# Kernel optimization log

Hardware: AMD Instinct MI355X
Metric: run time of the kernel (lower is better)

Reference implementation:

```python
import jax, jax.numpy as jnp
import numpy as np

B, T, D = 4, 2048, 1024
N_HEADS = 16
D_HEAD = D // N_HEADS


def setup_inputs() -> dict:
    key = jax.random.key(0)
    ks = jax.random.split(key, 5)
    s = 1.0 / np.sqrt(D)  # keep activations well-scaled
    return {
        "x": jax.random.normal(ks[0], (B, T, D), dtype=jnp.float32),
        "Wq": jax.random.normal(ks[1], (D, D), dtype=jnp.float32) * s,
        "Wk": jax.random.normal(ks[2], (D, D), dtype=jnp.float32) * s,
        "Wv": jax.random.normal(ks[3], (D, D), dtype=jnp.float32) * s,
        "Wo": jax.random.normal(ks[4], (D, D), dtype=jnp.float32) * s,
    }


def reference(x, Wq, Wk, Wv, Wo):
    Bx, Tx, C = x.shape
    # projections; nn.Linear(d,d,bias=False): y = x @ W^T
    def split_heads(y):
        return y.reshape(Bx, Tx, N_HEADS, D_HEAD).transpose(0, 2, 1, 3)  # [B,H,T,dh]
    q = split_heads(x @ Wq.T)
    k = split_heads(x @ Wk.T)
    v = split_heads(x @ Wv.T)
    scale = 1.0 / np.sqrt(D_HEAD)
    att = jnp.einsum("bhtd,bhsd->bhts", q, k) * scale  # [B,H,T,T]
    causal = jnp.tril(jnp.ones((Tx, Tx), dtype=bool))
    att = jnp.where(causal[None, None], att, -jnp.inf)
    att = jax.nn.softmax(att, axis=-1)
    y = jnp.einsum("bhts,bhsd->bhtd", att, v)  # [B,H,T,dh]
    y = y.transpose(0, 2, 1, 3).reshape(Bx, Tx, C)
    return y @ Wo.T
```

## Files before the change

### kernel.cpp

```cpp
#include <hip/hip_runtime.h>
#include <cstdint>
#include <cstddef>

typedef unsigned short u16;
typedef short bf16x8 __attribute__((ext_vector_type(8)));
typedef unsigned short u16x8 __attribute__((ext_vector_type(8)));
typedef float f32x4 __attribute__((ext_vector_type(4)));
typedef float f32x16 __attribute__((ext_vector_type(16)));
typedef unsigned u32x2 __attribute__((ext_vector_type(2)));

__device__ __forceinline__ u16 f2bf(float x) {
    union { float f; unsigned int u; } v; v.f = x;
    unsigned int u = v.u;
    unsigned int r = (u + 0x7fffu + ((u >> 16) & 1u)) >> 16;
    return (u16)r;
}

__device__ __forceinline__ unsigned cvtpk(float lo, float hi) {
    unsigned r;
    asm("v_cvt_pk_bf16_f32 %0, %1, %2" : "=v"(r) : "v"(lo), "v"(hi));
    return r;
}

__device__ __forceinline__ float exp2v(float x) {
    float y;
    asm("v_exp_f32 %0, %1" : "=v"(y) : "v"(x));
    return y;
}

__device__ __forceinline__ void load_lds16(const void* g, void* l) {
    __builtin_amdgcn_global_load_lds((const __attribute__((address_space(1))) void*)g,
                                     (__attribute__((address_space(3))) void*)l, 16, 0, 0);
}

__global__ void cast_f32_bf16(const float* __restrict__ in, u16* __restrict__ out, int n) {
    int i = (blockIdx.x * blockDim.x + threadIdx.x) * 4;
    int stride = gridDim.x * blockDim.x * 4;
    for (; i < n; i += stride) {
        float4 f = *reinterpret_cast<const float4*>(in + i);
        ushort4 o;
        o.x = f2bf(f.x); o.y = f2bf(f.y); o.z = f2bf(f.z); o.w = f2bf(f.w);
        *reinterpret_cast<ushort4*>(out + i) = o;
    }
}

__global__ void cast_w4(const float* __restrict__ w0, const float* __restrict__ w1,
                        const float* __restrict__ w2, const float* __restrict__ w3,
                        u16* __restrict__ out, int nw) {
    const int wsel = blockIdx.y;
    const float* in = (wsel == 0) ? w0 : (wsel == 1) ? w1 : (wsel == 2) ? w2 : w3;
    u16* o = out + (size_t)wsel * nw;
    int i = (blockIdx.x * blockDim.x + threadIdx.x) * 4;
    int stride = gridDim.x * blockDim.x * 4;
    for (; i < nw; i += stride) {
        float4 f = *reinterpret_cast<const float4*>(in + i);
        ushort4 v;
        v.x = f2bf(f.x); v.y = f2bf(f.y); v.z = f2bf(f.z); v.w = f2bf(f.w);
        *reinterpret_cast<ushort4*>(o + i) = v;
    }
}

__global__ __launch_bounds__(512, 2) void gemm_qkv(const u16* __restrict__ A,
                                                   const u16* __restrict__ Bw,
                                                   u16* __restrict__ qkout,
                                                   u16* __restrict__ vtg) {
    constexpr int K = 1024, NT = 32;
    __shared__ u16 smem[49152];

    const int tid  = threadIdx.x;
    const int m0   = blockIdx.x * 256;
    const int n0   = blockIdx.y * 256;
    const int wid  = tid >> 6, lane = tid & 63;
    const int fr   = lane & 15, g = lane >> 4;
    const int wm   = wid >> 2, wn = wid & 3;

    const int r0   = tid >> 2;
    const int ssrc = (tid & 3) ^ ((r0 >> 1) & 3);
    const int wb   = (tid & ~63) * 8;
    const u16* pA0 = A  + (size_t)(m0 + r0) * K + ssrc * 8;
    const u16* pA1 = A  + (size_t)(m0 + r0 + 128) * K + ssrc * 8;
    const u16* pB0 = Bw + (size_t)(n0 + r0) * K + ssrc * 8;
    const u16* pB1 = Bw + (size_t)(n0 + r0 + 128) * K + ssrc * 8;

    int offA[8], offB[4];
#pragma unroll
    for (int mf = 0; mf < 8; ++mf) {
        const int row = wm * 128 + mf * 16 + fr;
        offA[mf] = row * 32 + (g ^ ((row >> 1) & 3)) * 8;
    }
#pragma unroll
    for (int nfr = 0; nfr < 4; ++nfr) {
        const int row = wn * 64 + nfr * 16 + fr;
        offB[nfr] = 8192 + row * 32 + (g ^ ((row >> 1) & 3)) * 8;
    }

    f32x4 acc[8][4];
#pragma unroll
    for (int i = 0; i < 8; ++i)
#pragma unroll
        for (int j = 0; j < 4; ++j) acc[i][j] = f32x4{0.f, 0.f, 0.f, 0.f};

#define ISSUE(BUF) {                                                   \
        load_lds16(pA0, &smem[(BUF) * 16384 + wb]);                    \
        load_lds16(pA1, &smem[(BUF) * 16384 + 4096 + wb]);             \
        load_lds16(pB0, &smem[(BUF) * 16384 + 8192 + wb]);             \
        load_lds16(pB1, &smem[(BUF) * 16384 + 12288 + wb]);            \
        pA0 += 32; pA1 += 32; pB0 += 32; pB1 += 32; }

    ISSUE(0);
    ISSUE(1);

    int b = 0;
    for (int t = 0; t < NT; ++t) {
        if (t < NT - 1) asm volatile("s_waitcnt vmcnt(4)\n\ts_barrier" ::: "memory");
        else            asm volatile("s_waitcnt vmcnt(0)\n\ts_barrier" ::: "memory");

        if (t + 2 < NT) {
            const int b2 = (b == 0) ? 2 : b - 1;
            ISSUE(b2);
        }

        const u16* Tb = &smem[b * 16384];
        bf16x8 a[8], bv[4];
#pragma unroll
        for (int mf = 0; mf < 8; ++mf)
            a[mf] = *reinterpret_cast<const bf16x8*>(&Tb[offA[mf]]);
#pragma unroll
        for (int nfr = 0; nfr < 4; ++nfr)
            bv[nfr] = *reinterpret_cast<const bf16x8*>(&Tb[offB[nfr]]);

        __builtin_amdgcn_s_setprio(1);
#pragma unroll
        for (int mf = 0; mf < 8; ++mf)
#pragma unroll
            for (int nfr = 0; nfr < 4; ++nfr)
                acc[mf][nfr] = __builtin_amdgcn_mfma_f32_16x16x32_bf16(
                    a[mf], bv[nfr], acc[mf][nfr], 0, 0, 0);
        __builtin_amdgcn_s_setprio(0);

        b = (b == 2) ? 0 : b + 1;
    }
#undef ISSUE

    __syncthreads();

    char* sb = reinterpret_cast<char*>(smem);
    if (n0 < 2048) {
        const float osc = (n0 < 1024) ? 0.18033688011112042f : 1.0f;
#pragma unroll
        for (int half = 0; half < 2; ++half) {
            if (wm == half) {
#pragma unroll
                for (int mf = 0; mf < 8; ++mf)
#pragma unroll
                    for (int nfr = 0; nfr < 4; ++nfr) {
                        const int rl  = mf * 16 + g * 4;
                        const int col = wn * 64 + nfr * 16 + fr;
#pragma unroll
                        for (int i = 0; i < 4; ++i) {
                            const int row  = rl + i;
                            const int byte = row * 512 + ((col * 2) ^ (((row >> 2) & 3) << 5));
                            *reinterpret_cast<u16*>(sb + byte) = f2bf(acc[mf][nfr][i] * osc);
                        }
                    }
            }
            __syncthreads();
            {
                const int row = tid >> 2;
                const int swz = ((row >> 2) & 3) << 5;
#pragma unroll
                for (int p = 0; p < 8; ++p) {
                    const int sl   = (tid & 3) + p * 4;
                    const int byte = row * 512 + ((sl * 16) ^ swz);
                    u16x8 v = *reinterpret_cast<const u16x8*>(sb + byte);
                    *reinterpret_cast<u16x8*>(
                        &qkout[(size_t)(m0 + half * 128 + row) * 2048 + n0 + sl * 8]) = v;
                }
            }
            __syncthreads();
        }
    } else {
        const int bb = m0 >> 11, tloc = m0 & 2047;
#pragma unroll
        for (int half = 0; half < 2; ++half) {
            if ((wn >> 1) == half) {
#pragma unroll
                for (int mf = 0; mf < 8; ++mf)
#pragma unroll
                    for (int nfr = 0; nfr < 4; ++nfr) {
                        const int nl  = (wn & 1) * 64 + nfr * 16 + fr;
                        const int ml0 = wm * 128 + mf * 16 + g * 4;
                        const int f   = ((nl & 3) << 5) | (((nl >> 2) & 1) << 4);
                        uint2 pk;
                        pk.x = cvtpk(acc[mf][nfr][0], acc[mf][nfr][1]);
                        pk.y = cvtpk(acc[mf][nfr][2], acc[mf][nfr][3]);
                        *reinterpret_cast<uint2*>(sb + nl * 512 + ((ml0 * 2) ^ f)) = pk;
                    }
            }
            __syncthreads();
            {
                const int nl = tid >> 2;
                const int f  = ((nl & 3) << 5) | (((nl >> 2) & 1) << 4);
#pragma unroll
                for (int p = 0; p < 8; ++p) {
                    const int sl   = (tid & 3) + p * 4;
                    const int byte = nl * 512 + ((sl * 16) ^ f);
                    u16x8 v = *reinterpret_cast<const u16x8*>(sb + byte);
                    *reinterpret_cast<u16x8*>(
                        &vtg[(size_t)(bb * 1024 + (n0 - 2048) + half * 128 + nl) * 2048 +
                             tloc + sl * 8]) = v;
                }
            }
            __syncthreads();
        }
    }
}

__global__ __launch_bounds__(256) void gemm_out(const u16* __restrict__ A,
                                                const u16* __restrict__ Bw,
                                                float* __restrict__ C,
                                                int M, int N, int K) {
    __shared__ u16 smem[16384];
    u16* As = smem;
    u16* Bs = smem + 4096;

    const int tid  = threadIdx.x;
    const int m0   = blockIdx.x * 128;
    const int n0   = blockIdx.y * 128;
    const int wid  = tid >> 6;
    const int lane = tid & 63;
    const int wr   = (wid >> 1) * 64;
    const int wc   = (wid & 1) * 64;
    const int fr   = lane & 15;
    const int ko   = (lane >> 4) * 8;
    const int rq   = (lane >> 4) * 4;

    f32x4 acc[4][4];
#pragma unroll
    for (int i = 0; i < 4; ++i)
#pragma unroll
        for (int j = 0; j < 4; ++j) acc[i][j] = f32x4{0.f, 0.f, 0.f, 0.f};

    const int lr4 = lane >> 2;
    const int ls  = lane & 3;

    for (int k0 = 0; k0 < K; k0 += 32) {
#pragma unroll
        for (int t = 0; t < 2; ++t) {
            const int qtr = wid * 2 + t;
            const int r   = qtr * 16 + lr4;
            load_lds16(&A[(size_t)(m0 + r) * K + k0 + ls * 8], &As[qtr * 512]);
            load_lds16(&Bw[(size_t)(n0 + r) * K + k0 + ls * 8], &Bs[qtr * 512]);
        }
        __syncthreads();

        bf16x8 af[4], bfr[4];
#pragma unroll
        for (int mf = 0; mf < 4; ++mf)
            af[mf] = *reinterpret_cast<const bf16x8*>(&As[(wr + mf * 16 + fr) * 32 + ko]);
#pragma unroll
        for (int nf = 0; nf < 4; ++nf)
            bfr[nf] = *reinterpret_cast<const bf16x8*>(&Bs[(wc + nf * 16 + fr) * 32 + ko]);
        __builtin_amdgcn_s_setprio(1);
#pragma unroll
        for (int mf = 0; mf < 4; ++mf)
#pragma unroll
            for (int nf = 0; nf < 4; ++nf)
                acc[mf][nf] = __builtin_amdgcn_mfma_f32_16x16x32_bf16(
                    af[mf], bfr[nf], acc[mf][nf], 0, 0, 0);
        __builtin_amdgcn_s_setprio(0);
        __syncthreads();
    }

#pragma unroll
    for (int mf = 0; mf < 4; ++mf)
#pragma unroll
        for (int nf = 0; nf < 4; ++nf)
#pragma unroll
            for (int i = 0; i < 4; ++i)
                C[(size_t)(m0 + wr + mf * 16 + rq + i) * N + n0 + wc + nf * 16 + fr] =
                    acc[mf][nf][i];
}

__global__ __launch_bounds__(128) void attn_fwd(const u16* __restrict__ qk,
                                                const u16* __restrict__ vtg,
                                                u16* __restrict__ Y) {
    constexpr int T = 2048, DQK = 2048, DOUT = 1024;
    const int bh = blockIdx.x;
    const int jb = blockIdx.y;
    const int b  = bh >> 4, hd = bh & 15;
    const int tid = threadIdx.x, w = tid >> 6, lane = tid & 63;
    const int qloc = lane & 31, h2 = lane >> 5;

    __shared__ u16 Ks[2][4096];
    __shared__ u16 Vs[2][4096];

    const size_t rowb = (size_t)b * T;
    const int sr8 = lane >> 3, ss = lane & 7;
    const int sc = (ss ^ sr8) * 8;

#define BUILD_PA(sv, RB, dst) {                                               \
        unsigned wa  = cvtpk(sv[RB + 0], sv[RB + 1]);                         \
        unsigned wb2 = cvtpk(sv[RB + 2], sv[RB + 3]);                         \
        unsigned wc2 = cvtpk(sv[RB + 4], sv[RB + 5]);                         \
        unsigned wd  = cvtpk(sv[RB + 6], sv[RB + 7]);                         \
        u32x2 r0 = __builtin_amdgcn_permlane32_swap(wa, wc2, false, false);   \
        u32x2 r1 = __builtin_amdgcn_permlane32_swap(wb2, wd, false, false);   \
        dst.x = r0.x; dst.y = r1.x; dst.z = r0.y; dst.w = r1.y; }

#define PV_STEP(pa, KS, ROWBASE, oacc) {                                      \
        const int rr_ = (ROWBASE) + qloc;                                     \
        bf16x8 vf_ = *reinterpret_cast<const bf16x8*>(                        \
            &Vb[rr_ * 64 + (((2 * (KS) + h2) ^ (rr_ & 7)) * 8)]);             \
        oacc = __builtin_amdgcn_mfma_f32_32x32x16_bf16(                       \
            *reinterpret_cast<const bf16x8*>(&pa), vf_, oacc, 0, 0, 0); }

    for (int qi = 0; qi < 2; ++qi) {
        const int qt = (qi == 0) ? (31 - jb) : jb;
        const int q0 = qt * 64;
        const int wq = q0 + w * 32;
        const int NT = qt + 1;

        bf16x8 qf[4];
#pragma unroll
        for (int ks = 0; ks < 4; ++ks)
            qf[ks] = *reinterpret_cast<const bf16x8*>(
                &qk[(rowb + wq + qloc) * DQK + hd * 64 + ks * 16 + h2 * 8]);

        f32x16 o0, o1;
#pragma unroll
        for (int i = 0; i < 16; ++i) { o0[i] = 0.f; o1[i] = 0.f; }
        float lp = 0.f;

        const u16* kp[4];
        const u16* vp[4];
#pragma unroll
        for (int t = 0; t < 4; ++t) {
            const int r = (w * 4 + t) * 8 + sr8;
            kp[t] = qk + (rowb + r) * DQK + 1024 + hd * 64 + sc;
            vp[t] = vtg + ((size_t)bh * 64 + r) * T + sc;
        }

        __syncthreads();

#pragma unroll
        for (int t = 0; t < 4; ++t) {
            const int chunk = w * 4 + t;
            load_lds16(kp[t], &Ks[0][chunk * 512]);
            load_lds16(vp[t], &Vs[0][chunk * 512]);
        }
#pragma unroll
        for (int t = 0; t < 4; ++t) { kp[t] += 64 * DQK; vp[t] += 64; }

        for (int kt = 0; kt < NT; ++kt) {
            __syncthreads();

            if (kt + 1 < NT) {
                const int nb = (kt + 1) & 1;
#pragma unroll
                for (int t = 0; t < 4; ++t) {
                    const int chunk = w * 4 + t;
                    load_lds16(kp[t], &Ks[nb][chunk * 512]);
                    load_lds16(vp[t], &Vs[nb][chunk * 512]);
                }
#pragma unroll
                for (int t = 0; t < 4; ++t) { kp[t] += 64 * DQK; vp[t] += 64; }
            }

            const int k0 = kt * 64;
            if (k0 <= wq + 31) {
                const u16* Kb = Ks[kt & 1];
                const u16* Vb = Vs[kt & 1];
                const bool do1 = (k0 + 32 <= wq + 31);
                const bool dm  = (k0 + 63 > wq);

                f32x16 st0, st1;
#pragma unroll
                for (int i = 0; i < 16; ++i) { st0[i] = 0.f; st1[i] = 0.f; }

                __builtin_amdgcn_s_setprio(1);
#pragma unroll
                for (int ks = 0; ks < 4; ++ks) {
                    bf16x8 kf = *reinterpret_cast<const bf16x8*>(
                        &Kb[qloc * 64 + (((2 * ks + h2) ^ (qloc & 7)) * 8)]);
                    st0 = __builtin_amdgcn_mfma_f32_32x32x16_bf16(kf, qf[ks], st0, 0, 0, 0);
                }
                if (do1) {
#pragma unroll
                    for (int ks = 0; ks < 4; ++ks) {
                        const int r1 = 32 + qloc;
                        bf16x8 kf = *reinterpret_cast<const bf16x8*>(
                            &Kb[r1 * 64 + (((2 * ks + h2) ^ (r1 & 7)) * 8)]);
                        st1 = __builtin_amdgcn_mfma_f32_32x32x16_bf16(kf, qf[ks], st1, 0, 0, 0);
                    }
                }
                __builtin_amdgcn_s_setprio(0);

                const int qg = wq + qloc;
#pragma unroll
                for (int i = 0; i < 16; ++i) st0[i] = exp2v(st0[i]);
                if (do1) {
#pragma unroll
                    for (int i = 0; i < 16; ++i) st1[i] = exp2v(st1[i]);
                }
                if (dm) {
#pragma unroll
                    for (int r = 0; r < 16; ++r) {
                        const int crow = (r & 3) + 8 * (r >> 2) + 4 * h2;
                        if (k0 + crow > qg)      st0[r] = 0.f;
                        if (k0 + 32 + crow > qg) st1[r] = 0.f;
                    }
                }
                {
                    float l0 = 0.f, l1 = 0.f, l2 = 0.f, l3 = 0.f;
#pragma unroll
                    for (int i = 0; i < 4; ++i) {
                        l0 += st0[i]; l1 += st0[4 + i]; l2 += st0[8 + i]; l3 += st0[12 + i];
                    }
                    if (do1) {
#pragma unroll
                        for (int i = 0; i < 4; ++i) {
                            l0 += st1[i]; l1 += st1[4 + i]; l2 += st1[8 + i]; l3 += st1[12 + i];
                        }
                    }
                    lp += (l0 + l1) + (l2 + l3);
                }

                uint4 pa0, pa1, pa2, pa3;
                BUILD_PA(st0, 0, pa0);
                BUILD_PA(st0, 8, pa1);
                if (do1) {
                    BUILD_PA(st1, 0, pa2);
                    BUILD_PA(st1, 8, pa3);
                }

                __builtin_amdgcn_s_setprio(1);
                PV_STEP(pa0, 0, 0, o0);
                PV_STEP(pa1, 1, 0, o0);
                PV_STEP(pa0, 0, 32, o1);
                PV_STEP(pa1, 1, 32, o1);
                if (do1) {
                    PV_STEP(pa2, 2, 0, o0);
                    PV_STEP(pa3, 3, 0, o0);
                    PV_STEP(pa2, 2, 32, o1);
                    PV_STEP(pa3, 3, 32, o1);
                }
                __builtin_amdgcn_s_setprio(0);
            }
        }

        const float lf = lp + __shfl_xor(lp, 32);
        const float linv = 1.0f / lf;
#pragma unroll
        for (int r = 0; r < 16; ++r) {
            const int crow = (r & 3) + 8 * (r >> 2) + 4 * h2;
            const float rl = __shfl(linv, crow);
            const size_t yrow = rowb + wq + crow;
            Y[yrow * DOUT + hd * 64 + qloc]      = (u16)cvtpk(o0[r] * rl, 0.f);
            Y[yrow * DOUT + hd * 64 + 32 + qloc] = (u16)cvtpk(o1[r] * rl, 0.f);
        }
    }
#undef BUILD_PA
#undef PV_STEP
}

extern "C" void kernel_launch(void* const* d_in, const int* in_sizes, int n_in,
                              void* d_out, int out_size, void* d_ws, size_t ws_size,
                              hipStream_t stream) {
    const float* x  = (const float*)d_in[0];
    const float* Wq = (const float*)d_in[1];
    const float* Wk = (const float*)d_in[2];
    const float* Wv = (const float*)d_in[3];
    const float* Wo = (const float*)d_in[4];

    constexpr int B = 4, T = 2048, D = 1024;
    constexpr int M = B * T;
    const int nx = in_sizes[0];
    const int nw = in_sizes[1];

    char* ws = (char*)d_ws;
    u16* xb   = (u16*)(ws);
    u16* qkb  = (u16*)(ws + (16ull << 20));
    u16* vtg  = (u16*)(ws + (48ull << 20));
    u16* yb   = (u16*)(ws + (64ull << 20));
    u16* wqkv = (u16*)(ws + (80ull << 20));
    u16* wob  = wqkv + 3 * (size_t)nw;

    cast_f32_bf16<<<2048, 256, 0, stream>>>(x, xb, nx);
    cast_w4<<<dim3(256, 4), 256, 0, stream>>>(Wq, Wk, Wv, Wo, wqkv, nw);

    gemm_qkv<<<dim3(M / 256, 3072 / 256), 512, 0, stream>>>(xb, wqkv, qkb, vtg);

    attn_fwd<<<dim3(64, 16), 128, 0, stream>>>(qkb, vtg, yb);

    gemm_out<<<dim3(M / 128, D / 128), 256, 0, stream>>>(yb, wob, (float*)d_out, M, D, D);
}
```

Measured before the change: 169.6 us.

## Enlarge attention query tile to 256 rows with 8 waves sharing K/V tiles

```diff
diff --git a/kernel.cpp b/kernel.cpp
--- a/kernel.cpp
+++ b/kernel.cpp
@@ -282,7 +282,7 @@
                     acc[mf][nf][i];
 }
 
-__global__ __launch_bounds__(128) void attn_fwd(const u16* __restrict__ qk,
+__global__ __launch_bounds__(512) void attn_fwd(const u16* __restrict__ qk,
                                                 const u16* __restrict__ vtg,
                                                 u16* __restrict__ Y) {
     constexpr int T = 2048, DQK = 2048, DOUT = 1024;
@@ -296,8 +296,15 @@
     __shared__ u16 Vs[2][4096];
 
     const size_t rowb = (size_t)b * T;
-    const int sr8 = lane >> 3, ss = lane & 7;
-    const int sc = (ss ^ sr8) * 8;
+
+    const int srow = tid >> 3;
+    const int sc   = ((tid & 7) ^ (srow & 7)) * 8;
+    const int ldst = w * 512;
+
+    int off[4];
+#pragma unroll
+    for (int ks = 0; ks < 4; ++ks)
+        off[ks] = qloc * 64 + (((2 * ks + h2) ^ (qloc & 7)) * 8);
 
 #define BUILD_PA(sv, RB, dst) {                                               \
         unsigned wa  = cvtpk(sv[RB + 0], sv[RB + 1]);                         \
@@ -308,18 +315,16 @@
         u32x2 r1 = __builtin_amdgcn_permlane32_swap(wb2, wd, false, false);   \
         dst.x = r0.x; dst.y = r1.x; dst.z = r0.y; dst.w = r1.y; }
 
-#define PV_STEP(pa, KS, ROWBASE, oacc) {                                      \
-        const int rr_ = (ROWBASE) + qloc;                                     \
-        bf16x8 vf_ = *reinterpret_cast<const bf16x8*>(                        \
-            &Vb[rr_ * 64 + (((2 * (KS) + h2) ^ (rr_ & 7)) * 8)]);             \
+#define PV_STEP(pa, KS, RBOFF, oacc) {                                        \
+        bf16x8 vf_ = *reinterpret_cast<const bf16x8*>(&Vb[off[KS] + (RBOFF)]); \
         oacc = __builtin_amdgcn_mfma_f32_32x32x16_bf16(                       \
             *reinterpret_cast<const bf16x8*>(&pa), vf_, oacc, 0, 0, 0); }
 
     for (int qi = 0; qi < 2; ++qi) {
-        const int qt = (qi == 0) ? (31 - jb) : jb;
-        const int q0 = qt * 64;
+        const int qt = (qi == 0) ? (7 - jb) : jb;
+        const int q0 = qt * 256;
         const int wq = q0 + w * 32;
-        const int NT = qt + 1;
+        const int NT = 4 * qt + 4;
 
         bf16x8 qf[4];
 #pragma unroll
@@ -332,39 +337,23 @@
         for (int i = 0; i < 16; ++i) { o0[i] = 0.f; o1[i] = 0.f; }
         float lp = 0.f;
 
-        const u16* kp[4];
-        const u16* vp[4];
-#pragma unroll
-        for (int t = 0; t < 4; ++t) {
-            const int r = (w * 4 + t) * 8 + sr8;
-            kp[t] = qk + (rowb + r) * DQK + 1024 + hd * 64 + sc;
-            vp[t] = vtg + ((size_t)bh * 64 + r) * T + sc;
-        }
+        const u16* kp = qk  + (rowb + srow) * DQK + 1024 + hd * 64 + sc;
+        const u16* vp = vtg + ((size_t)bh * 64 + srow) * T + sc;
 
         __syncthreads();
 
-#pragma unroll
-        for (int t = 0; t < 4; ++t) {
-            const int chunk = w * 4 + t;
-            load_lds16(kp[t], &Ks[0][chunk * 512]);
-            load_lds16(vp[t], &Vs[0][chunk * 512]);
-        }
-#pragma unroll
-        for (int t = 0; t < 4; ++t) { kp[t] += 64 * DQK; vp[t] += 64; }
+        load_lds16(kp, &Ks[0][ldst]);
+        load_lds16(vp, &Vs[0][ldst]);
+        kp += 64 * DQK; vp += 64;
 
         for (int kt = 0; kt < NT; ++kt) {
             __syncthreads();
 
             if (kt + 1 < NT) {
                 const int nb = (kt + 1) & 1;
-#pragma unroll
-                for (int t = 0; t < 4; ++t) {
-                    const int chunk = w * 4 + t;
-                    load_lds16(kp[t], &Ks[nb][chunk * 512]);
-                    load_lds16(vp[t], &Vs[nb][chunk * 512]);
-                }
-#pragma unroll
-                for (int t = 0; t < 4; ++t) { kp[t] += 64 * DQK; vp[t] += 64; }
+                load_lds16(kp, &Ks[nb][ldst]);
+                load_lds16(vp, &Vs[nb][ldst]);
+                kp += 64 * DQK; vp += 64;
             }
 
             const int k0 = kt * 64;
@@ -381,16 +370,13 @@
                 __builtin_amdgcn_s_setprio(1);
 #pragma unroll
                 for (int ks = 0; ks < 4; ++ks) {
-                    bf16x8 kf = *reinterpret_cast<const bf16x8*>(
-                        &Kb[qloc * 64 + (((2 * ks + h2) ^ (qloc & 7)) * 8)]);
+                    bf16x8 kf = *reinterpret_cast<const bf16x8*>(&Kb[off[ks]]);
                     st0 = __builtin_amdgcn_mfma_f32_32x32x16_bf16(kf, qf[ks], st0, 0, 0, 0);
                 }
                 if (do1) {
 #pragma unroll
                     for (int ks = 0; ks < 4; ++ks) {
-                        const int r1 = 32 + qloc;
-                        bf16x8 kf = *reinterpret_cast<const bf16x8*>(
-                            &Kb[r1 * 64 + (((2 * ks + h2) ^ (r1 & 7)) * 8)]);
+                        bf16x8 kf = *reinterpret_cast<const bf16x8*>(&Kb[off[ks] + 2048]);
                         st1 = __builtin_amdgcn_mfma_f32_32x32x16_bf16(kf, qf[ks], st1, 0, 0, 0);
                     }
                 }
@@ -437,13 +423,13 @@
                 __builtin_amdgcn_s_setprio(1);
                 PV_STEP(pa0, 0, 0, o0);
                 PV_STEP(pa1, 1, 0, o0);
-                PV_STEP(pa0, 0, 32, o1);
-                PV_STEP(pa1, 1, 32, o1);
+                PV_STEP(pa0, 0, 2048, o1);
+                PV_STEP(pa1, 1, 2048, o1);
                 if (do1) {
                     PV_STEP(pa2, 2, 0, o0);
                     PV_STEP(pa3, 3, 0, o0);
-                    PV_STEP(pa2, 2, 32, o1);
-                    PV_STEP(pa3, 3, 32, o1);
+                    PV_STEP(pa2, 2, 2048, o1);
+                    PV_STEP(pa3, 3, 2048, o1);
                 }
                 __builtin_amdgcn_s_setprio(0);
             }
@@ -491,7 +477,7 @@
 
     gemm_qkv<<<dim3(M / 256, 3072 / 256), 512, 0, stream>>>(xb, wqkv, qkb, vtg);
 
-    attn_fwd<<<dim3(64, 16), 128, 0, stream>>>(qkb, vtg, yb);
+    attn_fwd<<<dim3(64, 4), 512, 0, stream>>>(qkb, vtg, yb);
 
     gemm_out<<<dim3(M / 128, D / 128), 256, 0, stream>>>(yb, wob, (float*)d_out, M, D, D);
 }
```

Measured after the change: 167.2 us. About the same (-1.4%).
